# Kernel tuning notes

Measured on AMD Instinct MI355X. Metric: run time of the kernel, lower is better.

The kernel has to match this reference:

```python
import jax, jax.numpy as jnp
import numpy as np

# Concrete func with analytic derivatives: f(x,a,b) = sigmoid(a*x + b)
# s' = s(1-s); s'' = s(1-s)(1-2s); s''' = s(1-s)(1-6s+6s^2)

def setup_inputs() -> dict:
    key = jax.random.key(0)
    k1, k2, k3, k4, k5 = jax.random.split(key, 5)
    B, N = 2048, 8192
    return {
        "x": jax.random.normal(k1, (B, N), dtype=jnp.float32),
        "a": jax.random.uniform(k2, (B, 1), dtype=jnp.float32) + 0.5,
        "b": jax.random.normal(k3, (B, 1), dtype=jnp.float32) * 0.1,
        "mean": jax.random.uniform(k4, (B, 1), dtype=jnp.float32),
        "var": jax.random.uniform(k5, (B, 1), dtype=jnp.float32) * 0.1,
        "dim": 1,
    }


def reference(x, a, b, mean, var, dim):
    ax = dim
    m = lambda t: jnp.mean(t, axis=ax, keepdims=True)

    u = a * x + b
    s = jax.nn.sigmoid(u)
    sp = s * (1.0 - s)            # f'
    spp = sp * (1.0 - 2.0 * s)    # f''

    f = s
    df_da = sp * x
    df_db = sp
    d2f_da2 = spp * x * x
    d2f_dab = spp * x
    d2f_db2 = spp

    fm = m(f)
    em = fm - mean
    dem_da = m(df_da)
    dem_db = m(df_db)
    d2em_da2 = m(d2f_da2)
    d2em_dab = m(d2f_dab)
    d2em_db2 = m(d2f_db2)

    ev = m(f * f) - fm ** 2 - var
    dev_da = 2 * (m(f * df_da) - fm * dem_da)
    dev_db = 2 * (m(f * df_db) - fm * dem_db)
    d2ev_da2 = 2 * (m(df_da ** 2 + f * d2f_da2) - dem_da ** 2 - fm * d2em_da2)
    d2ev_dab = 2 * (m(df_da * df_db + f * d2f_dab) - dem_da * dem_db - fm * d2em_dab)
    d2ev_db2 = 2 * (m(df_db ** 2 + f * d2f_db2) - dem_db ** 2 - fm * d2em_db2)

    dl_da = 2 * (em * dem_da + ev * dev_da)
    dl_db = 2 * (em * dem_db + ev * dev_db)
    d2l_da2 = 2 * (dem_da ** 2 + em * d2em_da2 + dev_da ** 2 + ev * d2ev_da2)
    d2l_dab = 2 * (dem_da * dem_db + em * d2em_dab + dev_da * dev_db + ev * d2ev_dab)
    d2l_db2 = 2 * (dem_db ** 2 + em * d2em_db2 + dev_db ** 2 + ev * d2ev_db2)

    den = d2l_da2 * d2l_db2 - d2l_dab ** 2
    na = (dl_da * d2l_db2 - dl_db * d2l_dab) / den
    nb = (dl_db * d2l_da2 - dl_da * d2l_dab) / den
    return (na, nb)
```

## Files before the change

### kernel.cpp

```cpp
#include <hip/hip_runtime.h>
#include <cmath>


#define THREADS 256

__device__ __forceinline__ float fast_exp2(float t) {
#if __has_builtin(__builtin_amdgcn_exp2f)
    return __builtin_amdgcn_exp2f(t);
#else
    return exp2f(t);
#endif
}

__device__ __forceinline__ float fast_rcp(float t) {
#if __has_builtin(__builtin_amdgcn_rcpf)
    return __builtin_amdgcn_rcpf(t);
#else
    return 1.0f / t;
#endif
}

__global__ __launch_bounds__(THREADS) void nsab_kernel(
    const float* __restrict__ x,
    const float* __restrict__ a,
    const float* __restrict__ b,
    const float* __restrict__ meanp,
    const float* __restrict__ varp,
    float* __restrict__ out,
    int B, int N)
{
    const int row = blockIdx.x;
    const int tid = threadIdx.x;

    const float av = a[row];
    const float bv = b[row];
    const float LOG2E = 1.4426950408889634f;
    const float c1 = -av * LOG2E;
    const float c0 = -bv * LOG2E;

    const float4* __restrict__ xr = (const float4*)(x + (size_t)row * (size_t)N);
    const int nvec = N >> 2;

    float a_s = 0.f, a_ss = 0.f, a_sp = 0.f, a_spx = 0.f;
    float a_q = 0.f, a_qx = 0.f, a_qx2 = 0.f;
    float a_fsp = 0.f, a_fspx = 0.f;
    float a_w = 0.f, a_wx = 0.f, a_wx2 = 0.f;

    #define NSAB_PROC(xx_)  do {                                        \
        const float xx  = (xx_);                                        \
        const float e   = fast_exp2(fmaf(c1, xx, c0));                  \
        const float s   = fast_rcp(1.0f + e);                           \
        const float sp  = s * (1.0f - s);                               \
        const float spp = sp * fmaf(-2.0f, s, 1.0f);                    \
        const float ssp = s * sp;                                       \
        const float w   = fmaf(s, spp, sp * sp);                        \
        const float x2  = xx * xx;                                      \
        a_s   += s;                                                     \
        a_ss   = fmaf(s,   s,   a_ss);                                  \
        a_sp  += sp;                                                    \
        a_spx  = fmaf(sp,  xx,  a_spx);                                 \
        a_q   += spp;                                                   \
        a_qx   = fmaf(spp, xx,  a_qx);                                  \
        a_qx2  = fmaf(spp, x2,  a_qx2);                                 \
        a_fsp += ssp;                                                   \
        a_fspx = fmaf(ssp, xx,  a_fspx);                                \
        a_w   += w;                                                     \
        a_wx   = fmaf(w,   xx,  a_wx);                                  \
        a_wx2  = fmaf(w,   x2,  a_wx2);                                 \
    } while (0)

    int i = tid;
    for (; i + 3 * THREADS < nvec; i += 4 * THREADS) {
        float4 v0 = xr[i];
        float4 v1 = xr[i +     THREADS];
        float4 v2 = xr[i + 2 * THREADS];
        float4 v3 = xr[i + 3 * THREADS];
        NSAB_PROC(v0.x); NSAB_PROC(v0.y); NSAB_PROC(v0.z); NSAB_PROC(v0.w);
        NSAB_PROC(v1.x); NSAB_PROC(v1.y); NSAB_PROC(v1.z); NSAB_PROC(v1.w);
        NSAB_PROC(v2.x); NSAB_PROC(v2.y); NSAB_PROC(v2.z); NSAB_PROC(v2.w);
        NSAB_PROC(v3.x); NSAB_PROC(v3.y); NSAB_PROC(v3.z); NSAB_PROC(v3.w);
    }
    for (; i < nvec; i += THREADS) {
        float4 v = xr[i];
        NSAB_PROC(v.x); NSAB_PROC(v.y); NSAB_PROC(v.z); NSAB_PROC(v.w);
    }
    #undef NSAB_PROC

    float acc[12] = {a_s, a_ss, a_sp, a_spx, a_q, a_qx, a_qx2,
                     a_fsp, a_fspx, a_w, a_wx, a_wx2};

    #pragma unroll
    for (int k = 0; k < 12; ++k) {
        float v = acc[k];
        #pragma unroll
        for (int off = 32; off > 0; off >>= 1)
            v += __shfl_down(v, off, 64);
        acc[k] = v;
    }

    __shared__ float part[THREADS / 64][12];
    const int wave = tid >> 6;
    const int lane = tid & 63;
    if (lane == 0) {
        #pragma unroll
        for (int k = 0; k < 12; ++k) part[wave][k] = acc[k];
    }
    __syncthreads();

    if (tid == 0) {
        double S[12];
        #pragma unroll
        for (int k = 0; k < 12; ++k)
            S[k] = (double)part[0][k] + (double)part[1][k]
                 + (double)part[2][k] + (double)part[3][k];

        const double invN = 1.0 / (double)N;
        const double fm       = S[0]  * invN;
        const double mff      = S[1]  * invN;
        const double dem_db   = S[2]  * invN;
        const double dem_da   = S[3]  * invN;
        const double d2em_db2 = S[4]  * invN;
        const double d2em_dab = S[5]  * invN;
        const double d2em_da2 = S[6]  * invN;
        const double m_fdfb   = S[7]  * invN;
        const double m_fdfa   = S[8]  * invN;
        const double m_w      = S[9]  * invN;
        const double m_wx     = S[10] * invN;
        const double m_wx2    = S[11] * invN;

        const double mv = (double)meanp[row];
        const double vv = (double)varp[row];

        const double em = fm - mv;
        const double ev = mff - fm * fm - vv;
        const double dev_da = 2.0 * (m_fdfa - fm * dem_da);
        const double dev_db = 2.0 * (m_fdfb - fm * dem_db);
        const double d2ev_da2 = 2.0 * (m_wx2 - dem_da * dem_da - fm * d2em_da2);
        const double d2ev_dab = 2.0 * (m_wx  - dem_da * dem_db - fm * d2em_dab);
        const double d2ev_db2 = 2.0 * (m_w   - dem_db * dem_db - fm * d2em_db2);

        const double dl_da = 2.0 * (em * dem_da + ev * dev_da);
        const double dl_db = 2.0 * (em * dem_db + ev * dev_db);
        const double d2l_da2 = 2.0 * (dem_da * dem_da + em * d2em_da2
                                    + dev_da * dev_da + ev * d2ev_da2);
        const double d2l_dab = 2.0 * (dem_da * dem_db + em * d2em_dab
                                    + dev_da * dev_db + ev * d2ev_dab);
        const double d2l_db2 = 2.0 * (dem_db * dem_db + em * d2em_db2
                                    + dev_db * dev_db + ev * d2ev_db2);

        const double den = d2l_da2 * d2l_db2 - d2l_dab * d2l_dab;
        const double na = (dl_da * d2l_db2 - dl_db * d2l_dab) / den;
        const double nb = (dl_db * d2l_da2 - dl_da * d2l_dab) / den;

        out[row]     = (float)na;
        out[B + row] = (float)nb;
    }
}

extern "C" void kernel_launch(void* const* d_in, const int* in_sizes, int n_in,
                              void* d_out, int out_size, void* d_ws, size_t ws_size,
                              hipStream_t stream) {
    const float* x    = (const float*)d_in[0];
    const float* a    = (const float*)d_in[1];
    const float* b    = (const float*)d_in[2];
    const float* mean = (const float*)d_in[3];
    const float* var  = (const float*)d_in[4];
    const int B = in_sizes[1];
    const int N = in_sizes[0] / B;
    float* out = (float*)d_out;

    nsab_kernel<<<dim3(B), dim3(THREADS), 0, stream>>>(x, a, b, mean, var, out, B, N);
}
```

Measured before the change: 107.6 us.

## Accumulate sigmoid power moments and reconstruct derivative sums algebraically

Replaces the per-element sp/spp/w terms with raw power moments s, s^2, s^3, s^4, each weighted by 1, x and x^2. The required derivative means are then rebuilt in double precision as linear combinations of these moments. This trims per-element ALU work and swaps the 4-way unrolled load loop for a one-ahead software-prefetch loop with unroll 1. The risk is cancellation error in float accumulators when the polynomial combinations subtract nearly equal moments, and the prefetch loop exposes less memory-level parallelism per thread.

```diff
diff --git a/kernel.cpp b/kernel.cpp
--- a/kernel.cpp
+++ b/kernel.cpp
@@ -41,53 +41,41 @@
     const float4* __restrict__ xr = (const float4*)(x + (size_t)row * (size_t)N);
     const int nvec = N >> 2;
 
-    float a_s = 0.f, a_ss = 0.f, a_sp = 0.f, a_spx = 0.f;
-    float a_q = 0.f, a_qx = 0.f, a_qx2 = 0.f;
-    float a_fsp = 0.f, a_fspx = 0.f;
-    float a_w = 0.f, a_wx = 0.f, a_wx2 = 0.f;
+    float A1 = 0.f, A2 = 0.f, A3 = 0.f, A4 = 0.f;
+    float B1 = 0.f, B2 = 0.f, B3 = 0.f, B4 = 0.f;
+    float C1 = 0.f, C2 = 0.f, C3 = 0.f, C4 = 0.f;
 
     #define NSAB_PROC(xx_)  do {                                        \
-        const float xx  = (xx_);                                        \
-        const float e   = fast_exp2(fmaf(c1, xx, c0));                  \
-        const float s   = fast_rcp(1.0f + e);                           \
-        const float sp  = s * (1.0f - s);                               \
-        const float spp = sp * fmaf(-2.0f, s, 1.0f);                    \
-        const float ssp = s * sp;                                       \
-        const float w   = fmaf(s, spp, sp * sp);                        \
-        const float x2  = xx * xx;                                      \
-        a_s   += s;                                                     \
-        a_ss   = fmaf(s,   s,   a_ss);                                  \
-        a_sp  += sp;                                                    \
-        a_spx  = fmaf(sp,  xx,  a_spx);                                 \
-        a_q   += spp;                                                   \
-        a_qx   = fmaf(spp, xx,  a_qx);                                  \
-        a_qx2  = fmaf(spp, x2,  a_qx2);                                 \
-        a_fsp += ssp;                                                   \
-        a_fspx = fmaf(ssp, xx,  a_fspx);                                \
-        a_w   += w;                                                     \
-        a_wx   = fmaf(w,   xx,  a_wx);                                  \
-        a_wx2  = fmaf(w,   x2,  a_wx2);                                 \
+        const float xx = (xx_);                                         \
+        const float e  = fast_exp2(fmaf(c1, xx, c0));                   \
+        const float s  = fast_rcp(1.0f + e);                            \
+        const float s2 = s * s;                                         \
+        const float s3 = s2 * s;                                        \
+        const float s4 = s2 * s2;                                       \
+        const float x2 = xx * xx;                                       \
+        A1 += s;  A2 += s2;  A3 += s3;  A4 += s4;                       \
+        B1 = fmaf(s,  xx, B1);  B2 = fmaf(s2, xx, B2);                  \
+        B3 = fmaf(s3, xx, B3);  B4 = fmaf(s4, xx, B4);                  \
+        C1 = fmaf(s,  x2, C1);  C2 = fmaf(s2, x2, C2);                  \
+        C3 = fmaf(s3, x2, C3);  C4 = fmaf(s4, x2, C4);                  \
     } while (0)
 
     int i = tid;
-    for (; i + 3 * THREADS < nvec; i += 4 * THREADS) {
-        float4 v0 = xr[i];
-        float4 v1 = xr[i +     THREADS];
-        float4 v2 = xr[i + 2 * THREADS];
-        float4 v3 = xr[i + 3 * THREADS];
-        NSAB_PROC(v0.x); NSAB_PROC(v0.y); NSAB_PROC(v0.z); NSAB_PROC(v0.w);
-        NSAB_PROC(v1.x); NSAB_PROC(v1.y); NSAB_PROC(v1.z); NSAB_PROC(v1.w);
-        NSAB_PROC(v2.x); NSAB_PROC(v2.y); NSAB_PROC(v2.z); NSAB_PROC(v2.w);
-        NSAB_PROC(v3.x); NSAB_PROC(v3.y); NSAB_PROC(v3.z); NSAB_PROC(v3.w);
-    }
-    for (; i < nvec; i += THREADS) {
-        float4 v = xr[i];
-        NSAB_PROC(v.x); NSAB_PROC(v.y); NSAB_PROC(v.z); NSAB_PROC(v.w);
+    if (i < nvec) {
+        float4 cur = xr[i];
+        #pragma unroll 1
+        for (; i + THREADS < nvec; i += THREADS) {
+            float4 nxt = xr[i + THREADS];
+            NSAB_PROC(cur.x); NSAB_PROC(cur.y);
+            NSAB_PROC(cur.z); NSAB_PROC(cur.w);
+            cur = nxt;
+        }
+        NSAB_PROC(cur.x); NSAB_PROC(cur.y);
+        NSAB_PROC(cur.z); NSAB_PROC(cur.w);
     }
     #undef NSAB_PROC
 
-    float acc[12] = {a_s, a_ss, a_sp, a_spx, a_q, a_qx, a_qx2,
-                     a_fsp, a_fspx, a_w, a_wx, a_wx2};
+    float acc[12] = {A1, A2, A3, A4, B1, B2, B3, B4, C1, C2, C3, C4};
 
     #pragma unroll
     for (int k = 0; k < 12; ++k) {
@@ -115,18 +103,25 @@
                  + (double)part[2][k] + (double)part[3][k];
 
         const double invN = 1.0 / (double)N;
-        const double fm       = S[0]  * invN;
-        const double mff      = S[1]  * invN;
-        const double dem_db   = S[2]  * invN;
-        const double dem_da   = S[3]  * invN;
-        const double d2em_db2 = S[4]  * invN;
-        const double d2em_dab = S[5]  * invN;
-        const double d2em_da2 = S[6]  * invN;
-        const double m_fdfb   = S[7]  * invN;
-        const double m_fdfa   = S[8]  * invN;
-        const double m_w      = S[9]  * invN;
-        const double m_wx     = S[10] * invN;
-        const double m_wx2    = S[11] * invN;
+        const double M1 = S[0] * invN, M2 = S[1] * invN;
+        const double M3 = S[2] * invN, M4 = S[3] * invN;
+        const double X1 = S[4] * invN, X2 = S[5] * invN;
+        const double X3 = S[6] * invN, X4 = S[7] * invN;
+        const double Y1 = S[8] * invN, Y2 = S[9] * invN;
+        const double Y3 = S[10] * invN, Y4 = S[11] * invN;
+
+        const double fm       = M1;
+        const double mff      = M2;
+        const double dem_db   = M1 - M2;
+        const double dem_da   = X1 - X2;
+        const double d2em_db2 = M1 - 3.0 * M2 + 2.0 * M3;
+        const double d2em_dab = X1 - 3.0 * X2 + 2.0 * X3;
+        const double d2em_da2 = Y1 - 3.0 * Y2 + 2.0 * Y3;
+        const double m_fdfb   = M2 - M3;
+        const double m_fdfa   = X2 - X3;
+        const double m_w      = 2.0 * M2 - 5.0 * M3 + 3.0 * M4;
+        const double m_wx     = 2.0 * X2 - 5.0 * X3 + 3.0 * X4;
+        const double m_wx2    = 2.0 * Y2 - 5.0 * Y3 + 3.0 * Y4;
 
         const double mv = (double)meanp[row];
         const double vv = (double)varp[row];
@@ -135,7 +130,8 @@
         const double ev = mff - fm * fm - vv;
         const double dev_da = 2.0 * (m_fdfa - fm * dem_da);
         const double dev_db = 2.0 * (m_fdfb - fm * dem_db);
-        const double d2ev_da2 = 2.0 * (m_wx2 - dem_da * dem_da - fm * d2em_da2);
+        const double d2ev_da2 = 2.0 * (d2em_da2 >= 0 ? (m_wx2 - dem_da * dem_da - fm * d2em_da2)
+                                                     : (m_wx2 - dem_da * dem_da - fm * d2em_da2));
         const double d2ev_dab = 2.0 * (m_wx  - dem_da * dem_db - fm * d2em_dab);
         const double d2ev_db2 = 2.0 * (m_w   - dem_db * dem_db - fm * d2em_db2);
 
```

Measured after the change: 104.2 us. 3.2% less time.
